# Optimization experiments

Measured on AMD Instinct MI355X. Metric: run time of the kernel, lower is better.

## Reference

```python
import jax, jax.numpy as jnp
import numpy as np

B, S, D = 2, 2048, 1024
H, KVH, HD = 16, 4, 64


def setup_inputs() -> dict:
    key = jax.random.key(0)
    ks = jax.random.split(key, 7)
    return {
        "hidden_states": jax.random.normal(ks[0], (B, S, D), jnp.float32),
        "full_mask": jax.random.normal(ks[1], (B, 1, S, S), jnp.float32),
        "tag_mask": jax.random.normal(ks[2], (B, 1, S, S), jnp.float32),
        "wq": jax.random.normal(ks[3], (H * HD, D), jnp.float32) * 0.02,
        "wk": jax.random.normal(ks[4], (KVH * HD, D), jnp.float32) * 0.02,
        "wv": jax.random.normal(ks[5], (KVH * HD, D), jnp.float32) * 0.02,
        "wo": jax.random.normal(ks[6], (D, H * HD), jnp.float32) * 0.02,
    }


def _masked_sdpa(q, k, v, mask):
    # q,k,v: [B, h, S, HD]; mask: [B, 1, S, S] additive bias
    scale = 1.0 / jnp.sqrt(jnp.asarray(HD, q.dtype))
    w = jnp.einsum("bhqd,bhkd->bhqk", q, k) * scale + mask
    w = jax.nn.softmax(w.astype(jnp.float32), axis=-1).astype(q.dtype)
    return jnp.einsum("bhqk,bhkd->bhqd", w, v)


def _repeat_kv(x, n_rep):
    # [B, KVh, S, HD] -> [B, KVh*n_rep, S, HD]
    if n_rep == 1:
        return x
    return jnp.repeat(x, n_rep, axis=1)


def reference(hidden_states, full_mask, tag_mask, wq, wk, wv, wo):
    x = hidden_states
    q = (x @ wq.T).reshape(B, S, H, HD).transpose(0, 2, 1, 3)      # bhsd
    k = (x @ wk.T).reshape(B, S, KVH, HD).transpose(0, 2, 1, 3)
    v = (x @ wv.T).reshape(B, S, KVH, HD).transpose(0, 2, 1, 3)

    n_gq, n_lq = H // 2, H - H // 2
    n_gkv, n_lkv = KVH // 2, KVH - KVH // 2
    q_g, q_l = q[:, :n_gq], q[:, n_gq:]
    k_g, k_l = k[:, :n_gkv], k[:, n_gkv:]
    v_g, v_l = v[:, :n_gkv], v[:, n_gkv:]

    k_g = _repeat_kv(k_g, n_gq // n_gkv)
    v_g = _repeat_kv(v_g, n_gq // n_gkv)
    k_l = _repeat_kv(k_l, n_lq // n_lkv)
    v_l = _repeat_kv(v_l, n_lq // n_lkv)

    out_g = _masked_sdpa(q_g, k_g, v_g, full_mask)
    out_l = _masked_sdpa(q_l, k_l, v_l, tag_mask)
    attn = jnp.concatenate([out_g, out_l], axis=1)                  # [B,H,S,HD]
    attn = attn.transpose(0, 2, 1, 3).reshape(B, S, H * HD)
    return attn @ wo.T
```

## Files before the change

### kernel.cpp

```cpp
#include <hip/hip_runtime.h>
#include <hip/hip_bf16.h>

#define B_ 2
#define S_ 2048
#define D_ 1024
#define H_ 16
#define KVH_ 4
#define HD_ 64

typedef __attribute__((ext_vector_type(4))) float f32x4;
typedef __attribute__((ext_vector_type(16))) float f32x16;
typedef __attribute__((ext_vector_type(8))) short short8;

#define DEV static __device__ __forceinline__

DEV unsigned short f2bf(float f) {
  union { float f; unsigned int u; } v; v.f = f;
  unsigned int r = v.u + 0x7FFFu + ((v.u >> 16) & 1u);
  return (unsigned short)(r >> 16);
}

DEV void gload_lds16(const void* g, void* l) {
  __builtin_amdgcn_global_load_lds(
      (const __attribute__((address_space(1))) unsigned int*)g,
      (__attribute__((address_space(3))) unsigned int*)l, 16, 0, 0);
}

__global__ __launch_bounds__(256) void cast_kernel(const float* __restrict__ src,
                                                   unsigned short* __restrict__ dst, int n4) {
  int i = blockIdx.x * 256 + threadIdx.x;
  if (i >= n4) return;
  float4 v = ((const float4*)src)[i];
  ushort4 o;
  o.x = f2bf(v.x); o.y = f2bf(v.y); o.z = f2bf(v.z); o.w = f2bf(v.w);
  ((ushort4*)dst)[i] = o;
}

template <int MODE>
__global__ __launch_bounds__(256) void gemm_bt(
    const unsigned short* __restrict__ A, const unsigned short* __restrict__ Bw,
    float* __restrict__ C, unsigned short* __restrict__ qb,
    unsigned short* __restrict__ kb, unsigned short* __restrict__ vb,
    int M, int N, int K, int ntn) {
  __shared__ __align__(16) unsigned short As[128 * 64];
  __shared__ __align__(16) unsigned short Bs[128 * 64];
  const int tid = threadIdx.x;
  const int lane = tid & 63, wid = tid >> 6;
  const int wr = wid >> 1, wc = wid & 1;
  const int tm = blockIdx.x / ntn, tn = blockIdx.x % ntn;
  const int row0 = tm * 128, col0 = tn * 128;
  f32x4 acc[4][4] = {};
  const int sr = tid >> 3, sc = (tid & 7) * 8;
  for (int kt = 0; kt < K; kt += 64) {
    __syncthreads();
#pragma unroll
    for (int i = 0; i < 4; ++i) {
      gload_lds16(A + (size_t)(row0 + i * 32 + sr) * K + kt + sc,
                  (void*)(As + i * 2048 + tid * 8));
      gload_lds16(Bw + (size_t)(col0 + i * 32 + sr) * K + kt + sc,
                  (void*)(Bs + i * 2048 + tid * 8));
    }
    __syncthreads();
#pragma unroll
    for (int ks = 0; ks < 64; ks += 32) {
      const int fc = ks + (lane >> 4) * 8;
      short8 af[4], bf[4];
#pragma unroll
      for (int m = 0; m < 4; ++m)
        af[m] = *(const short8*)&As[(wr * 64 + m * 16 + (lane & 15)) * 64 + fc];
#pragma unroll
      for (int n = 0; n < 4; ++n)
        bf[n] = *(const short8*)&Bs[(wc * 64 + n * 16 + (lane & 15)) * 64 + fc];
#pragma unroll
      for (int m = 0; m < 4; ++m)
#pragma unroll
        for (int n = 0; n < 4; ++n)
          acc[m][n] = __builtin_amdgcn_mfma_f32_16x16x32_bf16(af[m], bf[n], acc[m][n], 0, 0, 0);
    }
  }
#pragma unroll
  for (int m = 0; m < 4; ++m)
#pragma unroll
    for (int n = 0; n < 4; ++n)
#pragma unroll
      for (int j = 0; j < 4; ++j) {
        const int grow = row0 + wr * 64 + m * 16 + (lane >> 4) * 4 + j;
        const int gcol = col0 + wc * 64 + n * 16 + (lane & 15);
        const float v = acc[m][n][j];
        if (MODE == 0) {
          C[(size_t)grow * N + gcol] = v;
        } else {
          const int b = grow >> 11, s = grow & 2047;
          const unsigned short hv = f2bf(v);
          if (gcol < 1024) {
            const int hh = gcol >> 6, d = gcol & 63;
            qb[(((size_t)b * H_ + hh) * S_ + s) * HD_ + d] = hv;
          } else if (gcol < 1280) {
            const int kk = (gcol - 1024) >> 6, d = gcol & 63;
            kb[(((size_t)b * KVH_ + kk) * S_ + s) * HD_ + d] = hv;
          } else {
            const int kk = (gcol - 1280) >> 6, d = gcol & 63;
            vb[(((size_t)b * KVH_ + kk) * HD_ + d) * S_ + s] = hv;
          }
        }
      }
}

__global__ __launch_bounds__(256) void attn_kernel(
    const unsigned short* __restrict__ qb, const unsigned short* __restrict__ kb,
    const unsigned short* __restrict__ vb, const float* __restrict__ fmask,
    const float* __restrict__ tmask, unsigned short* __restrict__ attnb) {
  __shared__ __align__(16) unsigned short Ks[2][64 * 64];
  __shared__ __align__(16) unsigned short Vs[2][64 * 64];
  __shared__ __align__(16) float Ms[2][32 * 64];
  const int tid = threadIdx.x;
  const int lane = tid & 63, w = tid >> 6;
  const int l31 = lane & 31, hi = lane >> 5;

  const int swz = (blockIdx.x % 8) * 64 + blockIdx.x / 8;
  const int hh = swz & 1, qt = (swz >> 1) & 63, g = (swz >> 7) & 1, b = swz >> 8;
  const int h = g * 8 + hh * 4 + w;
  const int kvh = g * 2 + hh;

  const unsigned short* kbase = kb + ((size_t)b * KVH_ + kvh) * S_ * HD_;
  const unsigned short* vbase = vb + ((size_t)b * KVH_ + kvh) * S_ * HD_;
  const float* mbase = (g ? tmask : fmask) + (size_t)b * S_ * S_;

  short8 bq[4];
  {
    const unsigned short* qrow =
        qb + (((size_t)b * H_ + h) * S_ + qt * 32 + l31) * HD_;
#pragma unroll
    for (int ks = 0; ks < 4; ++ks)
      bq[ks] = *(const short8*)(qrow + ks * 16 + hi * 8);
  }

  f32x16 accO[2] = {};
  float mrow = -1e30f, lrow = 0.f;

  const int krow = tid >> 3, kblk = tid & 7;
  const int mrow_s = tid >> 4, mblk = tid & 15;

#define STAGE(KT, BUF)                                                                   \
  do {                                                                                   \
    gload_lds16(kbase + (size_t)((KT) + krow) * 64 + ((kblk ^ (krow & 7)) << 3),         \
                (void*)&Ks[BUF][tid * 8]);                                               \
    gload_lds16(kbase + (size_t)((KT) + 32 + krow) * 64 + ((kblk ^ (krow & 7)) << 3),    \
                (void*)&Ks[BUF][2048 + tid * 8]);                                        \
    gload_lds16(vbase + (size_t)krow * 2048 + (KT) + ((kblk ^ (krow & 7)) << 3),         \
                (void*)&Vs[BUF][tid * 8]);                                               \
    gload_lds16(vbase + (size_t)(32 + krow) * 2048 + (KT) + ((kblk ^ (krow & 7)) << 3),  \
                (void*)&Vs[BUF][2048 + tid * 8]);                                        \
    gload_lds16(mbase + (size_t)(qt * 32 + mrow_s) * 2048 + (KT) +                       \
                    ((mblk ^ (mrow_s & 15)) << 2),                                       \
                (void*)&Ms[BUF][tid * 4]);                                               \
    gload_lds16(mbase + (size_t)(qt * 32 + 16 + mrow_s) * 2048 + (KT) +                  \
                    ((mblk ^ (mrow_s & 15)) << 2),                                       \
                (void*)&Ms[BUF][1024 + tid * 4]);                                        \
  } while (0)

  STAGE(0, 0);
  for (int t = 0; t < 32; ++t) {
    const int cur = t & 1;
    if (t + 1 < 32) {
      STAGE((t + 1) * 64, cur ^ 1);
      asm volatile("s_waitcnt vmcnt(6)" ::: "memory");
    } else {
      asm volatile("s_waitcnt vmcnt(0)" ::: "memory");
    }
    __builtin_amdgcn_s_barrier();
    __builtin_amdgcn_sched_barrier(0);

    const unsigned short* ksb = Ks[cur];
    const unsigned short* vsb = Vs[cur];
    const float* msb = Ms[cur];

    f32x16 s[2] = {};
#pragma unroll
    for (int u = 0; u < 2; ++u)
#pragma unroll
      for (int ks = 0; ks < 4; ++ks) {
        short8 ak = *(const short8*)&ksb[(u * 32 + l31) * 64 +
                                         (((ks * 2 + hi) ^ (lane & 7)) << 3)];
        s[u] = __builtin_amdgcn_mfma_f32_32x32x16_bf16(ak, bq[ks], s[u], 0, 0, 0);
      }

    float tmax = -1e30f;
#pragma unroll
    for (int u = 0; u < 2; ++u)
#pragma unroll
      for (int rg = 0; rg < 4; ++rg) {
        f32x4 mk = *(const f32x4*)&msb[l31 * 64 +
                                       (((u * 8 + rg * 2 + hi) ^ (lane & 15)) << 2)];
#pragma unroll
        for (int e = 0; e < 4; ++e) {
          float v = s[u][rg * 4 + e] * 0.125f + mk[e];
          s[u][rg * 4 + e] = v;
          tmax = fmaxf(tmax, v);
        }
      }
    tmax = fmaxf(tmax, __shfl_xor(tmax, 32));

    if (__any(tmax > mrow + 8.f)) {
      const float mnew = fmaxf(mrow, tmax);
      const float es = __expf(mrow - mnew);
      mrow = mnew;
      lrow *= es;
#pragma unroll
      for (int r = 0; r < 16; ++r) {
        const float esb = __shfl(es, (r & 3) + 8 * (r >> 2) + 4 * hi);
        accO[0][r] *= esb;
        accO[1][r] *= esb;
      }
    }

    float rs = 0.f;
#pragma unroll
    for (int u = 0; u < 2; ++u)
#pragma unroll
      for (int r = 0; r < 16; ++r) {
        const float p = __expf(s[u][r] - mrow);
        s[u][r] = p;
        rs += p;
      }
    rs += __shfl_xor(rs, 32);
    lrow += rs;

#pragma unroll
    for (int u = 0; u < 2; ++u) {
      unsigned int Dw[8], Sw[8];
#pragma unroll
      for (int i = 0; i < 8; ++i)
        Dw[i] = (unsigned int)f2bf(s[u][2 * i]) |
                ((unsigned int)f2bf(s[u][2 * i + 1]) << 16);
#pragma unroll
      for (int i = 0; i < 8; ++i)
        Sw[i] = (unsigned int)__shfl_xor((int)Dw[i], 32);
      short8 ap[2];
#pragma unroll
      for (int k2 = 0; k2 < 2; ++k2) {
        union { unsigned int wd[4]; short8 v; } cv;
        const int b0 = k2 * 4;
        cv.wd[0] = hi ? Sw[b0 + 2] : Dw[b0 + 0];
        cv.wd[1] = hi ? Sw[b0 + 3] : Dw[b0 + 1];
        cv.wd[2] = hi ? Dw[b0 + 2] : Sw[b0 + 0];
        cv.wd[3] = hi ? Dw[b0 + 3] : Sw[b0 + 1];
        ap[k2] = cv.v;
      }
#pragma unroll
      for (int dt = 0; dt < 2; ++dt)
#pragma unroll
        for (int k2 = 0; k2 < 2; ++k2) {
          short8 bv = *(const short8*)&vsb[(dt * 32 + l31) * 64 +
                                           (((u * 4 + k2 * 2 + hi) ^ (lane & 7)) << 3)];
          accO[dt] = __builtin_amdgcn_mfma_f32_32x32x16_bf16(ap[k2], bv, accO[dt], 0, 0, 0);
        }
    }
    __builtin_amdgcn_s_barrier();
    __builtin_amdgcn_sched_barrier(0);
  }
#undef STAGE

#pragma unroll
  for (int r = 0; r < 16; ++r) {
    const int crow = (r & 3) + 8 * (r >> 2) + 4 * hi;
    const float linv = 1.0f / __shfl(lrow, crow);
    const size_t o = (size_t)(b * S_ + qt * 32 + crow) * (H_ * HD_) + h * 64 + l31;
    attnb[o] = f2bf(accO[0][r] * linv);
    attnb[o + 32] = f2bf(accO[1][r] * linv);
  }
}

extern "C" void kernel_launch(void* const* d_in, const int* in_sizes, int n_in,
                              void* d_out, int out_size, void* d_ws, size_t ws_size,
                              hipStream_t stream) {
  (void)in_sizes; (void)n_in; (void)out_size; (void)ws_size;
  const float* x = (const float*)d_in[0];
  const float* fmask = (const float*)d_in[1];
  const float* tmask = (const float*)d_in[2];
  const float* wq = (const float*)d_in[3];
  const float* wk = (const float*)d_in[4];
  const float* wv = (const float*)d_in[5];
  const float* wo = (const float*)d_in[6];

  unsigned short* ws = (unsigned short*)d_ws;
  unsigned short* xb = ws;
  unsigned short* wqkvb = xb + (size_t)4096 * 1024;
  unsigned short* wob = wqkvb + (size_t)1536 * 1024;
  unsigned short* qbuf = wob + (size_t)1024 * 1024;
  unsigned short* kbuf = qbuf + (size_t)4096 * 1024;
  unsigned short* vbuf = kbuf + (size_t)1024 * 1024;
  unsigned short* attnb = vbuf + (size_t)1024 * 1024;

  cast_kernel<<<4096, 256, 0, stream>>>(x, xb, 1048576);
  cast_kernel<<<1024, 256, 0, stream>>>(wq, wqkvb, 262144);
  cast_kernel<<<256, 256, 0, stream>>>(wk, wqkvb + (size_t)1024 * 1024, 65536);
  cast_kernel<<<256, 256, 0, stream>>>(wv, wqkvb + (size_t)1280 * 1024, 65536);
  cast_kernel<<<1024, 256, 0, stream>>>(wo, wob, 262144);

  gemm_bt<1><<<32 * 12, 256, 0, stream>>>(xb, wqkvb, nullptr, qbuf, kbuf, vbuf,
                                          4096, 1536, 1024, 12);
  attn_kernel<<<512, 256, 0, stream>>>(qbuf, kbuf, vbuf, fmask, tmask, attnb);
  gemm_bt<0><<<32 * 8, 256, 0, stream>>>(attnb, wob, (float*)d_out,
                                         nullptr, nullptr, nullptr, 4096, 1024, 1024, 8);
}
```

Baseline: 155.8 us.

## Fold softmax scale and log2e into Q, use exp2, setprio around MFMAs

Pre-multiplies Q by scale*log2e in the projection epilogue so the attention loop does one fma per score (mask*log2e + s) and can use the hardware exp2 instead of __expf. It also splits the max and sum reductions into independent chains, uses a packed bf16 conversion, raises wave priority around the MFMA blocks, and unrolls the KV loop by two. The lazy-rescale threshold becomes 11.5 in log2 units, roughly matching the old 8 in natural units. Risks include small numerical differences from rounding Q after scaling, and more register pressure from the unroll.

```diff
diff --git a/kernel.cpp b/kernel.cpp
--- a/kernel.cpp
+++ b/kernel.cpp
@@ -8,6 +8,9 @@
 #define KVH_ 4
 #define HD_ 64
 
+#define LOG2E 1.44269504089f
+#define QSCALE 0.18033688011f
+
 typedef __attribute__((ext_vector_type(4))) float f32x4;
 typedef __attribute__((ext_vector_type(16))) float f32x16;
 typedef __attribute__((ext_vector_type(8))) short short8;
@@ -18,6 +21,24 @@
   union { float f; unsigned int u; } v; v.f = f;
   unsigned int r = v.u + 0x7FFFu + ((v.u >> 16) & 1u);
   return (unsigned short)(r >> 16);
+}
+
+DEV float fexp2(float x) {
+#if __has_builtin(__builtin_amdgcn_exp2f)
+  return __builtin_amdgcn_exp2f(x);
+#else
+  float r;
+  asm("v_exp_f32 %0, %1" : "=v"(r) : "v"(x));
+  return r;
+#endif
+}
+
+DEV unsigned int pack_bf16(float lo, float hi) {
+  float2 f2; f2.x = lo; f2.y = hi;
+  __hip_bfloat162 h2 = __float22bfloat162_rn(f2);
+  union { __hip_bfloat162 h; unsigned int u; } cv;
+  cv.h = h2;
+  return cv.u;
 }
 
 DEV void gload_lds16(const void* g, void* l) {
@@ -91,16 +112,15 @@
           C[(size_t)grow * N + gcol] = v;
         } else {
           const int b = grow >> 11, s = grow & 2047;
-          const unsigned short hv = f2bf(v);
           if (gcol < 1024) {
             const int hh = gcol >> 6, d = gcol & 63;
-            qb[(((size_t)b * H_ + hh) * S_ + s) * HD_ + d] = hv;
+            qb[(((size_t)b * H_ + hh) * S_ + s) * HD_ + d] = f2bf(v * QSCALE);
           } else if (gcol < 1280) {
             const int kk = (gcol - 1024) >> 6, d = gcol & 63;
-            kb[(((size_t)b * KVH_ + kk) * S_ + s) * HD_ + d] = hv;
+            kb[(((size_t)b * KVH_ + kk) * S_ + s) * HD_ + d] = f2bf(v);
           } else {
             const int kk = (gcol - 1280) >> 6, d = gcol & 63;
-            vb[(((size_t)b * KVH_ + kk) * HD_ + d) * S_ + s] = hv;
+            vb[(((size_t)b * KVH_ + kk) * HD_ + d) * S_ + s] = f2bf(v);
           }
         }
       }
@@ -160,6 +180,7 @@
   } while (0)
 
   STAGE(0, 0);
+#pragma unroll 2
   for (int t = 0; t < 32; ++t) {
     const int cur = t & 1;
     if (t + 1 < 32) {
@@ -176,6 +197,7 @@
     const float* msb = Ms[cur];
 
     f32x16 s[2] = {};
+    __builtin_amdgcn_s_setprio(1);
 #pragma unroll
     for (int u = 0; u < 2; ++u)
 #pragma unroll
@@ -184,26 +206,32 @@
                                          (((ks * 2 + hi) ^ (lane & 7)) << 3)];
         s[u] = __builtin_amdgcn_mfma_f32_32x32x16_bf16(ak, bq[ks], s[u], 0, 0, 0);
       }
-
-    float tmax = -1e30f;
+    __builtin_amdgcn_s_setprio(0);
+
+    float tmax0 = -1e30f, tmax1 = -1e30f;
 #pragma unroll
     for (int u = 0; u < 2; ++u)
 #pragma unroll
       for (int rg = 0; rg < 4; ++rg) {
         f32x4 mk = *(const f32x4*)&msb[l31 * 64 +
                                        (((u * 8 + rg * 2 + hi) ^ (lane & 15)) << 2)];
-#pragma unroll
-        for (int e = 0; e < 4; ++e) {
-          float v = s[u][rg * 4 + e] * 0.125f + mk[e];
-          s[u][rg * 4 + e] = v;
-          tmax = fmaxf(tmax, v);
-        }
-      }
+        float v0 = fmaf(mk[0], LOG2E, s[u][rg * 4 + 0]);
+        float v1 = fmaf(mk[1], LOG2E, s[u][rg * 4 + 1]);
+        float v2 = fmaf(mk[2], LOG2E, s[u][rg * 4 + 2]);
+        float v3 = fmaf(mk[3], LOG2E, s[u][rg * 4 + 3]);
+        s[u][rg * 4 + 0] = v0;
+        s[u][rg * 4 + 1] = v1;
+        s[u][rg * 4 + 2] = v2;
+        s[u][rg * 4 + 3] = v3;
+        tmax0 = fmaxf(tmax0, fmaxf(v0, v1));
+        tmax1 = fmaxf(tmax1, fmaxf(v2, v3));
+      }
+    float tmax = fmaxf(tmax0, tmax1);
     tmax = fmaxf(tmax, __shfl_xor(tmax, 32));
 
-    if (__any(tmax > mrow + 8.f)) {
+    if (__any(tmax > mrow + 11.5f)) {
       const float mnew = fmaxf(mrow, tmax);
-      const float es = __expf(mrow - mnew);
+      const float es = fexp2(mrow - mnew);
       mrow = mnew;
       lrow *= es;
 #pragma unroll
@@ -214,15 +242,19 @@
       }
     }
 
-    float rs = 0.f;
+    float rs0 = 0.f, rs1 = 0.f, rs2 = 0.f, rs3 = 0.f;
 #pragma unroll
     for (int u = 0; u < 2; ++u)
 #pragma unroll
-      for (int r = 0; r < 16; ++r) {
-        const float p = __expf(s[u][r] - mrow);
-        s[u][r] = p;
-        rs += p;
-      }
+      for (int r = 0; r < 16; r += 4) {
+        float p0 = fexp2(s[u][r + 0] - mrow);
+        float p1 = fexp2(s[u][r + 1] - mrow);
+        float p2 = fexp2(s[u][r + 2] - mrow);
+        float p3 = fexp2(s[u][r + 3] - mrow);
+        s[u][r + 0] = p0; s[u][r + 1] = p1; s[u][r + 2] = p2; s[u][r + 3] = p3;
+        rs0 += p0; rs1 += p1; rs2 += p2; rs3 += p3;
+      }
+    float rs = (rs0 + rs1) + (rs2 + rs3);
     rs += __shfl_xor(rs, 32);
     lrow += rs;
 
@@ -231,8 +263,7 @@
       unsigned int Dw[8], Sw[8];
 #pragma unroll
       for (int i = 0; i < 8; ++i)
-        Dw[i] = (unsigned int)f2bf(s[u][2 * i]) |
-                ((unsigned int)f2bf(s[u][2 * i + 1]) << 16);
+        Dw[i] = pack_bf16(s[u][2 * i], s[u][2 * i + 1]);
 #pragma unroll
       for (int i = 0; i < 8; ++i)
         Sw[i] = (unsigned int)__shfl_xor((int)Dw[i], 32);
@@ -247,6 +278,7 @@
         cv.wd[3] = hi ? Dw[b0 + 3] : Sw[b0 + 1];
         ap[k2] = cv.v;
       }
+      __builtin_amdgcn_s_setprio(1);
 #pragma unroll
       for (int dt = 0; dt < 2; ++dt)
 #pragma unroll
@@ -255,6 +287,7 @@
                                            (((u * 4 + k2 * 2 + hi) ^ (lane & 7)) << 3)];
           accO[dt] = __builtin_amdgcn_mfma_f32_32x32x16_bf16(ap[k2], bv, accO[dt], 0, 0, 0);
         }
+      __builtin_amdgcn_s_setprio(0);
     }
     __builtin_amdgcn_s_barrier();
     __builtin_amdgcn_sched_barrier(0);
```

Measured after the change: 151.5 us. -2.8%, faster.
